# Performance work log

Hardware: AMD Instinct MI355X
Metric: run time of the kernel (lower is better)

Reference implementation:

```python
import jax, jax.numpy as jnp
import numpy as np

EPS = 1e-8


def setup_inputs() -> dict:
    key = jax.random.key(0)
    x = jax.random.normal(key, (16384, 1024), dtype=jnp.float32)
    return {"x": x}


def reference(x) -> jnp.ndarray:
    # L2 normalize along feature dim (torch F.normalize: x / max(||x||, eps))
    norm = jnp.linalg.norm(x, axis=-1, keepdims=True)
    xn = x / jnp.maximum(norm, EPS)

    n = xn.shape[0]
    # full pairwise cosine similarity [N, N]
    dot = xn @ xn.T
    # mask self-similarity on the diagonal
    ii = jnp.arange(n)
    dot = dot.at[ii, ii].set(-1.0)
    # nearest neighbor per row
    index = jnp.argmax(dot, axis=1)

    # torch PairwiseDistance(p=2, eps=1e-8): ||x1 - x2 + eps||_2
    diff = xn - xn[index] + EPS
    distances = jnp.linalg.norm(diff, axis=-1)

    loss = -jnp.mean(jnp.log(distances + EPS))
    return loss
```

## Files before the change

kernel.cpp:

```cpp
#include <hip/hip_runtime.h>
#include <math.h>

#define N 16384
#define D 1024
#define EPSF 1e-8f
#define QSCALE 448.0f
#define NPAIRS 2080
#define NBLK 256
#define PANB 262144
#define BIAS 16777216u

typedef __attribute__((ext_vector_type(4))) int i32x4;
typedef unsigned int u32;
typedef unsigned long long u64;

#define LDS_Bb 65536
#define LDS_TOT 131072

__device__ __forceinline__ void gload_lds16(const void* g, void* l) {
  __builtin_amdgcn_global_load_lds(
      (const __attribute__((address_space(1))) u32*)g,
      (__attribute__((address_space(3))) u32*)l, 16, 0, 0);
}

__device__ __forceinline__ int maxi(int x, int y) { return x > y ? x : y; }
__device__ __forceinline__ u32 maxu(u32 x, u32 y) { return x > y ? x : y; }

__device__ __forceinline__ void decode_pair(int t, int& a, int& b) {
  int aa = (int)((129.0 - sqrt(129.0 * 129.0 - 8.0 * (double)t)) * 0.5);
  if (aa < 0) aa = 0;
  if (aa > 63) aa = 63;
  while (((aa + 1) * 64 - ((aa + 1) * aa) / 2) <= t) ++aa;
  while ((aa * 64 - (aa * (aa - 1)) / 2) > t) --aa;
  a = aa;
  b = aa + (t - (aa * 64 - (aa * (aa - 1)) / 2));
}


__global__ __launch_bounds__(256) void k_normalize(
    const float* __restrict__ x, signed char* __restrict__ xq,
    float* __restrict__ norms, u64* __restrict__ best) {
  const int w = threadIdx.x >> 6, lane = threadIdx.x & 63;
  const int i = blockIdx.x * 4 + w;
  if (threadIdx.x < 4) best[(size_t)blockIdx.x * 4 + threadIdx.x] = 0;
  const float4* xi = (const float4*)(x + (size_t)i * D);
  float4 v[4];
  float s = 0.f;
#pragma unroll
  for (int t = 0; t < 4; ++t) {
    v[t] = xi[lane + t * 64];
    s += v[t].x * v[t].x + v[t].y * v[t].y + v[t].z * v[t].z + v[t].w * v[t].w;
  }
#pragma unroll
  for (int sh = 32; sh; sh >>= 1) s += __shfl_xor(s, sh, 64);
  const float nrm = sqrtf(s);
  if (lane == 0) norms[i] = nrm;
  const float qs = QSCALE / fmaxf(nrm, EPSF);
  u32* xo = (u32*)(xq + (size_t)i * D);
#pragma unroll
  for (int t = 0; t < 4; ++t) {
    const int q0 = __float2int_rn(fminf(fmaxf(v[t].x * qs, -127.f), 127.f));
    const int q1 = __float2int_rn(fminf(fmaxf(v[t].y * qs, -127.f), 127.f));
    const int q2 = __float2int_rn(fminf(fmaxf(v[t].z * qs, -127.f), 127.f));
    const int q3 = __float2int_rn(fminf(fmaxf(v[t].w * qs, -127.f), 127.f));
    xo[lane + t * 64] = (u32)(q0 & 0xff) | ((u32)(q1 & 0xff) << 8) |
                        ((u32)(q2 & 0xff) << 16) | ((u32)(q3 & 0xff) << 24);
  }
}


#define SGB(gaddr, daddr) \
  gload_lds16(xqB + (gaddr) + srcLane, lds + (daddr) + w * 1024)

#define STAGE2(T_, SLOT_)                                                \
  {                                                                      \
    const int t_ = (T_);                                                 \
    const int kt_ = t_ & 15;                                             \
    const size_t aG = (t_ >= 16 ? aPanN : aPan) + (size_t)(kt_ * 64);    \
    const size_t bG = (t_ >= 16 ? bPanN : bPan) + (size_t)(kt_ * 64);    \
    SGB(aG, (SLOT_)*16384);                                              \
    SGB(aG + 131072, (SLOT_)*16384 + 8192);                              \
    SGB(bG, LDS_Bb + (SLOT_)*16384);                                     \
    SGB(bG + 131072, LDS_Bb + (SLOT_)*16384 + 8192);                     \
  }

#define CTILE(SLOT_)                                                           \
  {                                                                            \
    i32x4 aa[4], bb[4];                                                        \
    _Pragma("unroll") for (int m = 0; m < 4; ++m) aa[m] =                      \
        *(const i32x4*)(lds + (SLOT_)*16384 + aOff[m]);                        \
    _Pragma("unroll") for (int n = 0; n < 4; ++n) bb[n] =                      \
        *(const i32x4*)(lds + LDS_Bb + (SLOT_)*16384 + bOff[n]);               \
    __builtin_amdgcn_s_setprio(1);                                             \
    _Pragma("unroll") for (int m = 0; m < 4; ++m)                              \
      _Pragma("unroll") for (int n = 0; n < 4; ++n)                            \
        acc[m][n] = __builtin_amdgcn_mfma_i32_16x16x64_i8(aa[m], bb[n],        \
                                                          acc[m][n], 0, 0, 0); \
    __builtin_amdgcn_s_setprio(0);                                             \
    _Pragma("unroll") for (int n = 0; n < 4; ++n) bb[n] =                      \
        *(const i32x4*)(lds + LDS_Bb + (SLOT_)*16384 + bOff[4 + n]);           \
    __builtin_amdgcn_s_setprio(1);                                             \
    _Pragma("unroll") for (int m = 0; m < 4; ++m)                              \
      _Pragma("unroll") for (int n = 0; n < 4; ++n)                            \
        acc[m][4 + n] = __builtin_amdgcn_mfma_i32_16x16x64_i8(                 \
            aa[m], bb[n], acc[m][4 + n], 0, 0, 0);                             \
    __builtin_amdgcn_s_setprio(0);                                             \
  }

#define GROUP(G_)                                                        \
  {                                                                      \
    __builtin_amdgcn_s_barrier();                                        \
    asm volatile("" ::: "memory");                                       \
    STAGE2(kq * 4 + 2 * (G_) + 2, 2 * ((G_) ^ 1));                       \
    STAGE2(kq * 4 + 2 * (G_) + 3, 2 * ((G_) ^ 1) + 1);                   \
    CTILE(2 * (G_));                                                     \
    CTILE(2 * (G_) + 1);                                                 \
    asm volatile("s_waitcnt vmcnt(0)" ::: "memory");                     \
  }

__global__ __launch_bounds__(512, 2) void k_argmax(
    const signed char* __restrict__ xq, u64* __restrict__ best) {
  extern __shared__ char lds[];
  const char* xqB = (const char*)xq;
  const int tid = (int)threadIdx.x, lane = tid & 63, w = tid >> 6;
  const int wr = w >> 1, wc = w & 1;

  int aOff[4], bOff[8];
  const int q = lane >> 4, li = lane & 15;
#pragma unroll
  for (int m = 0; m < 4; ++m) {
    const int rr = wr * 64 + m * 16 + li;
    const int line = rr >> 1;
    aOff[m] = line * 128 + ((((rr & 1) << 6) | (q << 4)) ^ ((line & 7) << 4));
  }
#pragma unroll
  for (int nf = 0; nf < 8; ++nf) {
    const int rr = wc * 128 + nf * 16 + li;
    const int line = rr >> 1;
    bOff[nf] = line * 128 + ((((rr & 1) << 6) | (q << 4)) ^ ((line & 7) << 4));
  }
  const int posx = (lane & 7) ^ (lane >> 3);
  const int rrl = ((w * 8 + (lane >> 3)) << 1) | (posx >> 2);
  const int srcLane = rrl * 1024 + (posx & 3) * 16;

  const int rB2 = wr * 64 + (q << 2);
  const int cB2 = wc * 128 + li;

  const int p0 = ((int)blockIdx.x * NPAIRS) / NBLK;
  const int p1 = (((int)blockIdx.x + 1) * NPAIRS) / NBLK;
  int a, b;
  decode_pair(p0, a, b);
  size_t aPan = (size_t)a * PANB, bPan = (size_t)b * PANB;
  size_t aPanN = aPan, bPanN = bPan;

  STAGE2(0, 0)
  STAGE2(1, 1)
  asm volatile("s_waitcnt vmcnt(0)" ::: "memory");

  i32x4 acc[4][8];
  for (int p = p0; p < p1; ++p) {
    int an = a, bn = b + 1;
    if (bn == 64) {
      an = a + 1;
      bn = an;
    }
    const bool lastp = (p == p1 - 1);
    aPanN = lastp ? aPan : (size_t)an * PANB;
    bPanN = lastp ? bPan : (size_t)bn * PANB;

#pragma unroll
    for (int m = 0; m < 4; ++m)
#pragma unroll
      for (int n = 0; n < 8; ++n) acc[m][n] = (i32x4){0, 0, 0, 0};

    for (int kq = 0; kq < 4; ++kq) {
      GROUP(0)
      GROUP(1)
    }

    const int aBase = a * 256, colBase = b * 256;
#pragma unroll
    for (int m = 0; m < 4; ++m)
#pragma unroll
      for (int r = 0; r < 4; ++r) {
        const int rl = rB2 + m * 16 + r;
        u32 pk = 0;
        if (a == b) {
#pragma unroll
          for (int nf = 0; nf < 8; ++nf) {
            u32 v = (((u32)acc[m][nf][r] + BIAS) << 7) | (u32)((nf << 4) | li);
            if (rl == cB2 + nf * 16) v = 0;
            pk = maxu(pk, v);
          }
        } else {
#pragma unroll
          for (int nf = 0; nf < 8; ++nf) {
            const u32 v =
                (((u32)acc[m][nf][r] + BIAS) << 7) | (u32)((nf << 4) | li);
            pk = maxu(pk, v);
          }
        }
#pragma unroll
        for (int sh = 1; sh < 16; sh <<= 1)
          pk = maxu(pk, (u32)__shfl_xor((int)pk, sh, 64));
        if (li == 0) {
          const int dot = (int)(pk >> 7) - (int)BIAS;
          const int col = colBase + wc * 128 + (int)(pk & 127u);
          const u64 key = ((u64)((u32)dot ^ 0x80000000u) << 32) | (u32)col;
          atomicMax(best + (aBase + rl), key);
        }
      }

    if (a != b) {
#pragma unroll
      for (int nf = 0; nf < 8; ++nf) {
        int pk = 0;
#pragma unroll
        for (int m = 0; m < 4; ++m)
#pragma unroll
          for (int r = 0; r < 4; ++r) {
            const int v = (int)((((u32)acc[m][nf][r] + BIAS) << 6) |
                                (u32)(m * 16 + q * 4 + r));
            pk = maxi(pk, v);
          }
        pk = maxi(pk, __shfl_xor(pk, 16, 64));
        pk = maxi(pk, __shfl_xor(pk, 32, 64));
        if (q == 0) {
          const int dot = (int)((((u32)pk) >> 6) - BIAS);
          const int grow = aBase + wr * 64 + (pk & 63);
          const u64 key = ((u64)((u32)dot ^ 0x80000000u) << 32) | (u32)grow;
          atomicMax(best + (colBase + cB2 + nf * 16), key);
        }
      }
    }

    a = an;
    b = bn;
    aPan = (size_t)a * PANB;
    bPan = (size_t)b * PANB;
  }
}


__global__ __launch_bounds__(256) void k_dist(
    const float* __restrict__ x, const float* __restrict__ norms,
    const u64* __restrict__ best, float* __restrict__ logd) {
  const int w = threadIdx.x >> 6, lane = threadIdx.x & 63;
  const int i = blockIdx.x * 4 + w;
  const u64 p = best[i];
  const int j = (int)(p & 0xffffffffu);
  const float invi = 1.f / fmaxf(norms[i], EPSF);
  const float invj = 1.f / fmaxf(norms[j], EPSF);
  const float4* xi = (const float4*)(x + (size_t)i * D);
  const float4* xj = (const float4*)(x + (size_t)j * D);
  float s = 0.f;
#pragma unroll
  for (int t = 0; t < 4; ++t) {
    const float4 av = xi[lane + t * 64], bv = xj[lane + t * 64];
    float d;
    d = av.x * invi - bv.x * invj + EPSF; s += d * d;
    d = av.y * invi - bv.y * invj + EPSF; s += d * d;
    d = av.z * invi - bv.z * invj + EPSF; s += d * d;
    d = av.w * invi - bv.w * invj + EPSF; s += d * d;
  }
#pragma unroll
  for (int sh = 32; sh; sh >>= 1) s += __shfl_xor(s, sh, 64);
  if (lane == 0) logd[i] = logf(sqrtf(s) + EPSF);
}


__global__ __launch_bounds__(256) void k_final(const float* __restrict__ logd,
                                               float* __restrict__ out) {
  __shared__ double red[256];
  double s = 0.0;
  for (int i = threadIdx.x; i < N; i += 256) s += (double)logd[i];
  red[threadIdx.x] = s;
  __syncthreads();
  for (int sh = 128; sh; sh >>= 1) {
    if ((int)threadIdx.x < sh) red[threadIdx.x] += red[threadIdx.x + sh];
    __syncthreads();
  }
  if (threadIdx.x == 0) out[0] = (float)(-red[0] / (double)N);
}


extern "C" void kernel_launch(void* const* d_in, const int* in_sizes, int n_in,
                              void* d_out, int out_size, void* d_ws,
                              size_t ws_size, hipStream_t stream) {
  const float* x = (const float*)d_in[0];
  float* out = (float*)d_out;
  char* ws = (char*)d_ws;

  signed char* xq = (signed char*)ws;
  float* norms = (float*)(ws + 16777216);
  u64* best = (u64*)(ws + 16842752);
  float* logd = (float*)(ws + 16973824);

  k_normalize<<<N / 4, 256, 0, stream>>>(x, xq, norms, best);
  k_argmax<<<NBLK, 512, LDS_TOT, stream>>>(xq, best);
  k_dist<<<N / 4, 256, 0, stream>>>(x, norms, best, logd);
  k_final<<<1, 256, 0, stream>>>(logd, out);
}
```

Baseline: 222.9 us.

## Split argmax tiles into 128x256 half-tiles with 256-thread blocks

Retiles the int8 similarity GEMM so each work item covers half of a 256x256 pair tile (128 rows by 256 columns), processed by 256-thread blocks with 512 blocks in total. The LDS pipeline becomes a two-slot, single-k-step double buffer of 48KB in place of a four-slot 128KB scheme. The aim is a better balance of work across CUs and higher occupancy. In exchange, B panels are loaded twice (once per half), barriers are more frequent, and there is less prefetch depth.

```diff
diff --git a/kernel.cpp b/kernel.cpp
--- a/kernel.cpp
+++ b/kernel.cpp
@@ -6,7 +6,8 @@
 #define EPSF 1e-8f
 #define QSCALE 448.0f
 #define NPAIRS 2080
-#define NBLK 256
+#define NT 4160
+#define NBLK 512
 #define PANB 262144
 #define BIAS 16777216u
 
@@ -14,8 +15,8 @@
 typedef unsigned int u32;
 typedef unsigned long long u64;
 
-#define LDS_Bb 65536
-#define LDS_TOT 131072
+#define SLOTB 24576
+#define LDS_TOT 49152
 
 __device__ __forceinline__ void gload_lds16(const void* g, void* l) {
   __builtin_amdgcn_global_load_lds(
@@ -72,25 +73,32 @@
 #define SGB(gaddr, daddr) \
   gload_lds16(xqB + (gaddr) + srcLane, lds + (daddr) + w * 1024)
 
-#define STAGE2(T_, SLOT_)                                                \
-  {                                                                      \
-    const int t_ = (T_);                                                 \
-    const int kt_ = t_ & 15;                                             \
-    const size_t aG = (t_ >= 16 ? aPanN : aPan) + (size_t)(kt_ * 64);    \
-    const size_t bG = (t_ >= 16 ? bPanN : bPan) + (size_t)(kt_ * 64);    \
-    SGB(aG, (SLOT_)*16384);                                              \
-    SGB(aG + 131072, (SLOT_)*16384 + 8192);                              \
-    SGB(bG, LDS_Bb + (SLOT_)*16384);                                     \
-    SGB(bG + 131072, LDS_Bb + (SLOT_)*16384 + 8192);                     \
-  }
-
-#define CTILE(SLOT_)                                                           \
+#define STG(aG_, bG_, SD_)                      \
+  {                                             \
+    SGB((aG_), (SD_));                          \
+    SGB((aG_) + 65536, (SD_) + 4096);           \
+    SGB((bG_), (SD_) + 8192);                   \
+    SGB((bG_) + 65536, (SD_) + 12288);          \
+    SGB((bG_) + 131072, (SD_) + 16384);         \
+    SGB((bG_) + 131072 + 65536, (SD_) + 20480); \
+  }
+
+#define KT(T_)                                                                 \
   {                                                                            \
+    const int t_ = (T_);                                                       \
+    const int tn_ = t_ + 1;                                                    \
+    const int ktn_ = tn_ & 15;                                                 \
+    const size_t aG = (tn_ >= 16 ? aPanHN : aPanH) + (size_t)(ktn_ * 64) + wG; \
+    const size_t bG = (tn_ >= 16 ? bPanN : bPan) + (size_t)(ktn_ * 64) + wG;   \
+    __builtin_amdgcn_s_barrier();                                              \
+    asm volatile("" ::: "memory");                                             \
+    STG(aG, bG, (tn_ & 1) * SLOTB);                                            \
+    const int sr = (t_ & 1) * SLOTB;                                           \
     i32x4 aa[4], bb[4];                                                        \
     _Pragma("unroll") for (int m = 0; m < 4; ++m) aa[m] =                      \
-        *(const i32x4*)(lds + (SLOT_)*16384 + aOff[m]);                        \
+        *(const i32x4*)(lds + sr + aOff[m]);                                   \
     _Pragma("unroll") for (int n = 0; n < 4; ++n) bb[n] =                      \
-        *(const i32x4*)(lds + LDS_Bb + (SLOT_)*16384 + bOff[n]);               \
+        *(const i32x4*)(lds + sr + 8192 + bOff[n]);                            \
     __builtin_amdgcn_s_setprio(1);                                             \
     _Pragma("unroll") for (int m = 0; m < 4; ++m)                              \
       _Pragma("unroll") for (int n = 0; n < 4; ++n)                            \
@@ -98,27 +106,17 @@
                                                           acc[m][n], 0, 0, 0); \
     __builtin_amdgcn_s_setprio(0);                                             \
     _Pragma("unroll") for (int n = 0; n < 4; ++n) bb[n] =                      \
-        *(const i32x4*)(lds + LDS_Bb + (SLOT_)*16384 + bOff[4 + n]);           \
+        *(const i32x4*)(lds + sr + 8192 + bOff[4 + n]);                        \
     __builtin_amdgcn_s_setprio(1);                                             \
     _Pragma("unroll") for (int m = 0; m < 4; ++m)                              \
       _Pragma("unroll") for (int n = 0; n < 4; ++n)                            \
         acc[m][4 + n] = __builtin_amdgcn_mfma_i32_16x16x64_i8(                 \
             aa[m], bb[n], acc[m][4 + n], 0, 0, 0);                             \
     __builtin_amdgcn_s_setprio(0);                                             \
-  }
-
-#define GROUP(G_)                                                        \
-  {                                                                      \
-    __builtin_amdgcn_s_barrier();                                        \
-    asm volatile("" ::: "memory");                                       \
-    STAGE2(kq * 4 + 2 * (G_) + 2, 2 * ((G_) ^ 1));                       \
-    STAGE2(kq * 4 + 2 * (G_) + 3, 2 * ((G_) ^ 1) + 1);                   \
-    CTILE(2 * (G_));                                                     \
-    CTILE(2 * (G_) + 1);                                                 \
-    asm volatile("s_waitcnt vmcnt(0)" ::: "memory");                     \
-  }
-
-__global__ __launch_bounds__(512, 2) void k_argmax(
+    asm volatile("s_waitcnt vmcnt(0)" ::: "memory");                           \
+  }
+
+__global__ __launch_bounds__(256, 2) void k_argmax(
     const signed char* __restrict__ xq, u64* __restrict__ best) {
   extern __shared__ char lds[];
   const char* xqB = (const char*)xq;
@@ -126,59 +124,62 @@
   const int wr = w >> 1, wc = w & 1;
 
   int aOff[4], bOff[8];
-  const int q = lane >> 4, li = lane & 15;
+  const int qh = lane >> 4, li = lane & 15;
 #pragma unroll
   for (int m = 0; m < 4; ++m) {
     const int rr = wr * 64 + m * 16 + li;
     const int line = rr >> 1;
-    aOff[m] = line * 128 + ((((rr & 1) << 6) | (q << 4)) ^ ((line & 7) << 4));
+    aOff[m] = line * 128 + ((((rr & 1) << 6) | (qh << 4)) ^ ((line & 7) << 4));
   }
 #pragma unroll
   for (int nf = 0; nf < 8; ++nf) {
     const int rr = wc * 128 + nf * 16 + li;
     const int line = rr >> 1;
-    bOff[nf] = line * 128 + ((((rr & 1) << 6) | (q << 4)) ^ ((line & 7) << 4));
+    bOff[nf] = line * 128 + ((((rr & 1) << 6) | (qh << 4)) ^ ((line & 7) << 4));
   }
   const int posx = (lane & 7) ^ (lane >> 3);
-  const int rrl = ((w * 8 + (lane >> 3)) << 1) | (posx >> 2);
-  const int srcLane = rrl * 1024 + (posx & 3) * 16;
-
-  const int rB2 = wr * 64 + (q << 2);
+  const int srcLane =
+      (((lane >> 3) << 1) | (posx >> 2)) * 1024 + (posx & 3) * 16;
+  const size_t wG = (size_t)w * 16384;
+
+  const int rB2 = wr * 64 + (qh << 2);
   const int cB2 = wc * 128 + li;
 
-  const int p0 = ((int)blockIdx.x * NPAIRS) / NBLK;
-  const int p1 = (((int)blockIdx.x + 1) * NPAIRS) / NBLK;
+  const int t0 = ((int)blockIdx.x * NT) / NBLK;
+  const int t1 = (((int)blockIdx.x + 1) * NT) / NBLK;
   int a, b;
-  decode_pair(p0, a, b);
-  size_t aPan = (size_t)a * PANB, bPan = (size_t)b * PANB;
-  size_t aPanN = aPan, bPanN = bPan;
-
-  STAGE2(0, 0)
-  STAGE2(1, 1)
+  decode_pair(t0 >> 1, a, b);
+  int half = t0 & 1;
+  size_t aPanH = (size_t)a * PANB + (size_t)half * 131072;
+  size_t bPan = (size_t)b * PANB;
+  size_t aPanHN = aPanH, bPanN = bPan;
+
+  STG(aPanH + wG, bPan + wG, 0);
   asm volatile("s_waitcnt vmcnt(0)" ::: "memory");
 
   i32x4 acc[4][8];
-  for (int p = p0; p < p1; ++p) {
-    int an = a, bn = b + 1;
-    if (bn == 64) {
-      an = a + 1;
-      bn = an;
+  for (int tt = t0; tt < t1; ++tt) {
+    const int ttn = (tt + 1 < t1) ? tt + 1 : tt;
+    int an, bn;
+    decode_pair(ttn >> 1, an, bn);
+    const int halfn = ttn & 1;
+    aPanHN = (size_t)an * PANB + (size_t)halfn * 131072;
+    bPanN = (size_t)bn * PANB;
+
+#pragma unroll
+    for (int m = 0; m < 4; ++m)
+#pragma unroll
+      for (int n = 0; n < 8; ++n) acc[m][n] = (i32x4){0, 0, 0, 0};
+
+    for (int kq = 0; kq < 4; ++kq) {
+      KT(kq * 4 + 0)
+      KT(kq * 4 + 1)
+      KT(kq * 4 + 2)
+      KT(kq * 4 + 3)
     }
-    const bool lastp = (p == p1 - 1);
-    aPanN = lastp ? aPan : (size_t)an * PANB;
-    bPanN = lastp ? bPan : (size_t)bn * PANB;
-
-#pragma unroll
-    for (int m = 0; m < 4; ++m)
-#pragma unroll
-      for (int n = 0; n < 8; ++n) acc[m][n] = (i32x4){0, 0, 0, 0};
-
-    for (int kq = 0; kq < 4; ++kq) {
-      GROUP(0)
-      GROUP(1)
-    }
-
-    const int aBase = a * 256, colBase = b * 256;
+
+    const int aBaseH = a * 256 + half * 128;
+    const int colBase = b * 256;
 #pragma unroll
     for (int m = 0; m < 4; ++m)
 #pragma unroll
@@ -186,10 +187,11 @@
         const int rl = rB2 + m * 16 + r;
         u32 pk = 0;
         if (a == b) {
+          const int rg = half * 128 + rl;
 #pragma unroll
           for (int nf = 0; nf < 8; ++nf) {
             u32 v = (((u32)acc[m][nf][r] + BIAS) << 7) | (u32)((nf << 4) | li);
-            if (rl == cB2 + nf * 16) v = 0;
+            if (rg == cB2 + nf * 16) v = 0;
             pk = maxu(pk, v);
           }
         } else {
@@ -207,7 +209,7 @@
           const int dot = (int)(pk >> 7) - (int)BIAS;
           const int col = colBase + wc * 128 + (int)(pk & 127u);
           const u64 key = ((u64)((u32)dot ^ 0x80000000u) << 32) | (u32)col;
-          atomicMax(best + (aBase + rl), key);
+          atomicMax(best + (aBaseH + rl), key);
         }
       }
 
@@ -220,14 +222,14 @@
 #pragma unroll
           for (int r = 0; r < 4; ++r) {
             const int v = (int)((((u32)acc[m][nf][r] + BIAS) << 6) |
-                                (u32)(m * 16 + q * 4 + r));
+                                (u32)(m * 16 + qh * 4 + r));
             pk = maxi(pk, v);
           }
         pk = maxi(pk, __shfl_xor(pk, 16, 64));
         pk = maxi(pk, __shfl_xor(pk, 32, 64));
-        if (q == 0) {
+        if (qh == 0) {
           const int dot = (int)((((u32)pk) >> 6) - BIAS);
-          const int grow = aBase + wr * 64 + (pk & 63);
+          const int grow = aBaseH + wr * 64 + (pk & 63);
           const u64 key = ((u64)((u32)dot ^ 0x80000000u) << 32) | (u32)grow;
           atomicMax(best + (colBase + cB2 + nf * 16), key);
         }
@@ -236,8 +238,9 @@
 
     a = an;
     b = bn;
-    aPan = (size_t)a * PANB;
-    bPan = (size_t)b * PANB;
+    half = halfn;
+    aPanH = aPanHN;
+    bPan = bPanN;
   }
 }
 
@@ -297,7 +300,7 @@
   float* logd = (float*)(ws + 16973824);
 
   k_normalize<<<N / 4, 256, 0, stream>>>(x, xq, norms, best);
-  k_argmax<<<NBLK, 512, LDS_TOT, stream>>>(xq, best);
+  k_argmax<<<NBLK, 256, LDS_TOT, stream>>>(xq, best);
   k_dist<<<N / 4, 256, 0, stream>>>(x, norms, best, logd);
   k_final<<<1, 256, 0, stream>>>(logd, out);
 }
```

Measured after the change: 235.1 us. 1.05x slower.

## Load A operand directly into registers from MFMA-ordered transposed copy

Applied to the files above, without the earlier changes.

The normalize kernel now also writes an int8 copy of the data laid out in 16-byte granules ordered by k-chunk and row, so the argmax GEMM can load A fragments straight from global memory into registers (double-buffered across k-steps) instead of staging them through LDS. Only B goes through LDS now, with a 4-slot ring and a finer per-k-step barrier and wait schedule, which halves LDS use. This removes LDS traffic and bank pressure for A, but adds an extra 16MB write in normalize, more global-load latency exposure per k-step and more VGPRs for the A buffers.

```diff
diff --git a/kernel.cpp b/kernel.cpp
--- a/kernel.cpp
+++ b/kernel.cpp
@@ -8,14 +8,14 @@
 #define NPAIRS 2080
 #define NBLK 256
 #define PANB 262144
+#define GRANB 262144
 #define BIAS 16777216u
 
 typedef __attribute__((ext_vector_type(4))) int i32x4;
 typedef unsigned int u32;
 typedef unsigned long long u64;
 
-#define LDS_Bb 65536
-#define LDS_TOT 131072
+#define LDS_TOT 65536
 
 __device__ __forceinline__ void gload_lds16(const void* g, void* l) {
   __builtin_amdgcn_global_load_lds(
@@ -39,7 +39,8 @@
 
 __global__ __launch_bounds__(256) void k_normalize(
     const float* __restrict__ x, signed char* __restrict__ xq,
-    float* __restrict__ norms, u64* __restrict__ best) {
+    signed char* __restrict__ xqT, float* __restrict__ norms,
+    u64* __restrict__ best) {
   const int w = threadIdx.x >> 6, lane = threadIdx.x & 63;
   const int i = blockIdx.x * 4 + w;
   if (threadIdx.x < 4) best[(size_t)blockIdx.x * 4 + threadIdx.x] = 0;
@@ -57,14 +58,18 @@
   if (lane == 0) norms[i] = nrm;
   const float qs = QSCALE / fmaxf(nrm, EPSF);
   u32* xo = (u32*)(xq + (size_t)i * D);
+  u32* xoT = (u32*)xqT;
 #pragma unroll
   for (int t = 0; t < 4; ++t) {
     const int q0 = __float2int_rn(fminf(fmaxf(v[t].x * qs, -127.f), 127.f));
     const int q1 = __float2int_rn(fminf(fmaxf(v[t].y * qs, -127.f), 127.f));
     const int q2 = __float2int_rn(fminf(fmaxf(v[t].z * qs, -127.f), 127.f));
     const int q3 = __float2int_rn(fminf(fmaxf(v[t].w * qs, -127.f), 127.f));
-    xo[lane + t * 64] = (u32)(q0 & 0xff) | ((u32)(q1 & 0xff) << 8) |
-                        ((u32)(q2 & 0xff) << 16) | ((u32)(q3 & 0xff) << 24);
+    const u32 val = (u32)(q0 & 0xff) | ((u32)(q1 & 0xff) << 8) |
+                    ((u32)(q2 & 0xff) << 16) | ((u32)(q3 & 0xff) << 24);
+    const int wrd = lane + t * 64;
+    xo[wrd] = val;
+    xoT[((size_t)(wrd >> 2) * 16384 + (u32)i) * 4 + (wrd & 3)] = val;
   }
 }
 
@@ -72,67 +77,62 @@
 #define SGB(gaddr, daddr) \
   gload_lds16(xqB + (gaddr) + srcLane, lds + (daddr) + w * 1024)
 
-#define STAGE2(T_, SLOT_)                                                \
-  {                                                                      \
-    const int t_ = (T_);                                                 \
-    const int kt_ = t_ & 15;                                             \
-    const size_t aG = (t_ >= 16 ? aPanN : aPan) + (size_t)(kt_ * 64);    \
-    const size_t bG = (t_ >= 16 ? bPanN : bPan) + (size_t)(kt_ * 64);    \
-    SGB(aG, (SLOT_)*16384);                                              \
-    SGB(aG + 131072, (SLOT_)*16384 + 8192);                              \
-    SGB(bG, LDS_Bb + (SLOT_)*16384);                                     \
-    SGB(bG + 131072, LDS_Bb + (SLOT_)*16384 + 8192);                     \
-  }
-
-#define CTILE(SLOT_)                                                           \
-  {                                                                            \
-    i32x4 aa[4], bb[4];                                                        \
-    _Pragma("unroll") for (int m = 0; m < 4; ++m) aa[m] =                      \
-        *(const i32x4*)(lds + (SLOT_)*16384 + aOff[m]);                        \
-    _Pragma("unroll") for (int n = 0; n < 4; ++n) bb[n] =                      \
-        *(const i32x4*)(lds + LDS_Bb + (SLOT_)*16384 + bOff[n]);               \
-    __builtin_amdgcn_s_setprio(1);                                             \
-    _Pragma("unroll") for (int m = 0; m < 4; ++m)                              \
-      _Pragma("unroll") for (int n = 0; n < 4; ++n)                            \
-        acc[m][n] = __builtin_amdgcn_mfma_i32_16x16x64_i8(aa[m], bb[n],        \
-                                                          acc[m][n], 0, 0, 0); \
-    __builtin_amdgcn_s_setprio(0);                                             \
-    _Pragma("unroll") for (int n = 0; n < 4; ++n) bb[n] =                      \
-        *(const i32x4*)(lds + LDS_Bb + (SLOT_)*16384 + bOff[4 + n]);           \
-    __builtin_amdgcn_s_setprio(1);                                             \
-    _Pragma("unroll") for (int m = 0; m < 4; ++m)                              \
-      _Pragma("unroll") for (int n = 0; n < 4; ++n)                            \
-        acc[m][4 + n] = __builtin_amdgcn_mfma_i32_16x16x64_i8(                 \
-            aa[m], bb[n], acc[m][4 + n], 0, 0, 0);                             \
-    __builtin_amdgcn_s_setprio(0);                                             \
-  }
-
-#define GROUP(G_)                                                        \
-  {                                                                      \
-    __builtin_amdgcn_s_barrier();                                        \
-    asm volatile("" ::: "memory");                                       \
-    STAGE2(kq * 4 + 2 * (G_) + 2, 2 * ((G_) ^ 1));                       \
-    STAGE2(kq * 4 + 2 * (G_) + 3, 2 * ((G_) ^ 1) + 1);                   \
-    CTILE(2 * (G_));                                                     \
-    CTILE(2 * (G_) + 1);                                                 \
-    asm volatile("s_waitcnt vmcnt(0)" ::: "memory");                     \
+#define KT1(K_, AC, AN)                                                       \
+  {                                                                           \
+    __builtin_amdgcn_s_barrier();                                             \
+    asm volatile("" ::: "memory");                                            \
+    if ((K_) < 15) {                                                          \
+      const char* aT = xqTB + aRowB + (size_t)(((K_) + 1) * 4) * GRANB;       \
+      AN[0] = *(const i32x4*)(aT);                                            \
+      AN[1] = *(const i32x4*)(aT + 256);                                      \
+      AN[2] = *(const i32x4*)(aT + 512);                                      \
+      AN[3] = *(const i32x4*)(aT + 768);                                      \
+    } else {                                                                  \
+      const char* aT = xqTB + aRowBN;                                         \
+      AN[0] = *(const i32x4*)(aT);                                            \
+      AN[1] = *(const i32x4*)(aT + 256);                                      \
+      AN[2] = *(const i32x4*)(aT + 512);                                      \
+      AN[3] = *(const i32x4*)(aT + 768);                                      \
+    }                                                                         \
+    {                                                                         \
+      const int t_ = (K_) + 3;                                                \
+      const int kt_ = t_ & 15;                                                \
+      const size_t bG = (t_ >= 16 ? bPanN : bPan) + (size_t)(kt_ * 64);       \
+      SGB(bG, (t_ & 3) * 16384);                                              \
+      SGB(bG + 131072, (t_ & 3) * 16384 + 8192);                              \
+    }                                                                         \
+    i32x4 bb[4];                                                              \
+    _Pragma("unroll") for (int n = 0; n < 4; ++n) bb[n] =                     \
+        *(const i32x4*)(lds + ((K_)&3) * 16384 + bOff[n]);                    \
+    __builtin_amdgcn_s_setprio(1);                                            \
+    _Pragma("unroll") for (int m = 0; m < 4; ++m)                             \
+      _Pragma("unroll") for (int n = 0; n < 4; ++n)                           \
+        acc[m][n] = __builtin_amdgcn_mfma_i32_16x16x64_i8(AC[m], bb[n],       \
+                                                          acc[m][n], 0, 0,    \
+                                                          0);                 \
+    __builtin_amdgcn_s_setprio(0);                                            \
+    _Pragma("unroll") for (int n = 0; n < 4; ++n) bb[n] =                     \
+        *(const i32x4*)(lds + ((K_)&3) * 16384 + bOff[4 + n]);                \
+    __builtin_amdgcn_s_setprio(1);                                            \
+    _Pragma("unroll") for (int m = 0; m < 4; ++m)                             \
+      _Pragma("unroll") for (int n = 0; n < 4; ++n)                           \
+        acc[m][4 + n] = __builtin_amdgcn_mfma_i32_16x16x64_i8(                \
+            AC[m], bb[n], acc[m][4 + n], 0, 0, 0);                            \
+    __builtin_amdgcn_s_setprio(0);                                            \
+    asm volatile("s_waitcnt vmcnt(6)" ::: "memory");                          \
   }
 
 __global__ __launch_bounds__(512, 2) void k_argmax(
-    const signed char* __restrict__ xq, u64* __restrict__ best) {
+    const signed char* __restrict__ xq, const signed char* __restrict__ xqT,
+    u64* __restrict__ best) {
   extern __shared__ char lds[];
   const char* xqB = (const char*)xq;
+  const char* xqTB = (const char*)xqT;
   const int tid = (int)threadIdx.x, lane = tid & 63, w = tid >> 6;
   const int wr = w >> 1, wc = w & 1;
 
-  int aOff[4], bOff[8];
+  int bOff[8];
   const int q = lane >> 4, li = lane & 15;
-#pragma unroll
-  for (int m = 0; m < 4; ++m) {
-    const int rr = wr * 64 + m * 16 + li;
-    const int line = rr >> 1;
-    aOff[m] = line * 128 + ((((rr & 1) << 6) | (q << 4)) ^ ((line & 7) << 4));
-  }
 #pragma unroll
   for (int nf = 0; nf < 8; ++nf) {
     const int rr = wc * 128 + nf * 16 + li;
@@ -150,12 +150,24 @@
   const int p1 = (((int)blockIdx.x + 1) * NPAIRS) / NBLK;
   int a, b;
   decode_pair(p0, a, b);
-  size_t aPan = (size_t)a * PANB, bPan = (size_t)b * PANB;
-  size_t aPanN = aPan, bPanN = bPan;
-
-  STAGE2(0, 0)
-  STAGE2(1, 1)
-  asm volatile("s_waitcnt vmcnt(0)" ::: "memory");
+  size_t bPan = (size_t)b * PANB;
+  size_t aRowB = (size_t)q * GRANB + (size_t)(a * 256 + wr * 64 + li) * 16;
+  size_t aRowBN = aRowB, bPanN = bPan;
+
+  i32x4 aaA[4], aaB[4];
+  {
+    const char* aT = xqTB + aRowB;
+    aaA[0] = *(const i32x4*)(aT);
+    aaA[1] = *(const i32x4*)(aT + 256);
+    aaA[2] = *(const i32x4*)(aT + 512);
+    aaA[3] = *(const i32x4*)(aT + 768);
+    aaB[0] = aaA[0]; aaB[1] = aaA[1]; aaB[2] = aaA[2]; aaB[3] = aaA[3];
+  }
+  for (int pp = 0; pp < 3; ++pp) {
+    SGB(bPan + (size_t)(pp * 64), pp * 16384);
+    SGB(bPan + (size_t)(pp * 64) + 131072, pp * 16384 + 8192);
+  }
+  asm volatile("s_waitcnt vmcnt(4)" ::: "memory");
 
   i32x4 acc[4][8];
   for (int p = p0; p < p1; ++p) {
@@ -165,18 +177,22 @@
       bn = an;
     }
     const bool lastp = (p == p1 - 1);
-    aPanN = lastp ? aPan : (size_t)an * PANB;
-    bPanN = lastp ? bPan : (size_t)bn * PANB;
+    if (lastp) {
+      an = a;
+      bn = b;
+    }
+    aRowBN = (size_t)q * GRANB + (size_t)(an * 256 + wr * 64 + li) * 16;
+    bPanN = (size_t)bn * PANB;
 
 #pragma unroll
     for (int m = 0; m < 4; ++m)
 #pragma unroll
       for (int n = 0; n < 8; ++n) acc[m][n] = (i32x4){0, 0, 0, 0};
 
-    for (int kq = 0; kq < 4; ++kq) {
-      GROUP(0)
-      GROUP(1)
-    }
+    KT1(0, aaA, aaB) KT1(1, aaB, aaA) KT1(2, aaA, aaB) KT1(3, aaB, aaA)
+    KT1(4, aaA, aaB) KT1(5, aaB, aaA) KT1(6, aaA, aaB) KT1(7, aaB, aaA)
+    KT1(8, aaA, aaB) KT1(9, aaB, aaA) KT1(10, aaA, aaB) KT1(11, aaB, aaA)
+    KT1(12, aaA, aaB) KT1(13, aaB, aaA) KT1(14, aaA, aaB) KT1(15, aaB, aaA)
 
     const int aBase = a * 256, colBase = b * 256;
 #pragma unroll
@@ -236,8 +252,8 @@
 
     a = an;
     b = bn;
-    aPan = (size_t)a * PANB;
-    bPan = (size_t)b * PANB;
+    aRowB = aRowBN;
+    bPan = bPanN;
   }
 }
 
@@ -292,12 +308,13 @@
   char* ws = (char*)d_ws;
 
   signed char* xq = (signed char*)ws;
-  float* norms = (float*)(ws + 16777216);
-  u64* best = (u64*)(ws + 16842752);
-  float* logd = (float*)(ws + 16973824);
-
-  k_normalize<<<N / 4, 256, 0, stream>>>(x, xq, norms, best);
-  k_argmax<<<NBLK, 512, LDS_TOT, stream>>>(xq, best);
+  signed char* xqT = (signed char*)(ws + 16777216);
+  float* norms = (float*)(ws + 33554432);
+  u64* best = (u64*)(ws + 33619968);
+  float* logd = (float*)(ws + 33751040);
+
+  k_normalize<<<N / 4, 256, 0, stream>>>(x, xq, xqT, norms, best);
+  k_argmax<<<NBLK, 512, LDS_TOT, stream>>>(xq, xqT, best);
   k_dist<<<N / 4, 256, 0, stream>>>(x, norms, best, logd);
   k_final<<<1, 256, 0, stream>>>(logd, out);
 }
```

Measured after the change: 242.2 us. 1.09x slower.
